# Kernel tuning notes

Measured on AMD Instinct MI355X. Metric: run time of the kernel, lower is better.

The kernel has to match this reference:

```python
import jax, jax.numpy as jnp
import numpy as np
from jax import lax

SCALES = [0.5, 0.25, 0.125, 0.0625]
D_MODEL = 256
IN_CH = 1


def setup_inputs() -> dict:
    key = jax.random.key(0)
    ks = jax.random.split(key, 16)
    x = jax.random.normal(ks[0], (2, D_MODEL, 256, 256), dtype=jnp.float32)
    m = jax.random.uniform(ks[1], (2, IN_CH, 256, 256), dtype=jnp.float32)
    s = 0.05
    Wq = jax.random.normal(ks[2], (D_MODEL, D_MODEL, 1, 1), jnp.float32) * s
    bq = jax.random.normal(ks[3], (D_MODEL,), jnp.float32) * s
    Wk = jax.random.normal(ks[4], (D_MODEL, D_MODEL, 1, 1), jnp.float32) * s
    bk = jax.random.normal(ks[5], (D_MODEL,), jnp.float32) * s
    Wv = jax.random.normal(ks[6], (D_MODEL, D_MODEL, 1, 1), jnp.float32) * s
    bv = jax.random.normal(ks[7], (D_MODEL,), jnp.float32) * s
    Wmq = jax.random.normal(ks[8], (D_MODEL, IN_CH, 1, 1), jnp.float32) * s
    bmq = jax.random.normal(ks[9], (D_MODEL,), jnp.float32) * s
    Wmk = jax.random.normal(ks[10], (D_MODEL, IN_CH, 1, 1), jnp.float32) * s
    bmk = jax.random.normal(ks[11], (D_MODEL,), jnp.float32) * s
    Wo = jax.random.normal(ks[12], (D_MODEL, D_MODEL, 3, 3), jnp.float32) * s
    bo = jax.random.normal(ks[13], (D_MODEL,), jnp.float32) * s
    return {"x": x, "m": m, "Wq": Wq, "bq": bq, "Wk": Wk, "bk": bk,
            "Wv": Wv, "bv": bv, "Wmq": Wmq, "bmq": bmq, "Wmk": Wmk, "bmk": bmk,
            "Wo": Wo, "bo": bo, "b": 1, "c": 256}


def _conv1x1(z, W, bias):
    # W: (O, I, 1, 1)
    return jnp.einsum('bihw,oi->bohw', z, W[:, :, 0, 0]) + bias[None, :, None, None]


def _forward(x, m, Wq, bq, Wk, bk, Wv, bv, Wmq, bmq, Wmk, bmk, Wo, bo, b, c):
    bt, _, h, w = x.shape  # h, w are multiples of 64 -> pad is zero
    t = bt // b
    n_scales = len(SCALES)
    d_k = c // n_scales

    q = _conv1x1(x, Wq, bq)
    k = _conv1x1(x, Wk, bk)
    v = _conv1x1(x, Wv, bv)
    mq = _conv1x1(m, Wmq, bmq)
    mk = _conv1x1(m, Wmk, bmk)

    outs = []
    for i, scale in enumerate(SCALES):
        height, width = int(h * scale), int(w * scale)
        out_h, out_w = h // height, w // width
        sl = slice(i * d_k, (i + 1) * d_k)

        def patch(z):
            # (b, t, d_k, out_h, height, out_w, width) -> (b, t*out_h*out_w, d_k*height*width)
            z = z[:, sl].reshape(b, t, d_k, out_h, height, out_w, width)
            z = z.transpose(0, 1, 3, 5, 2, 4, 6)
            return z.reshape(b, t * out_h * out_w, d_k * height * width)

        Q, K, V = patch(q), patch(k), patch(v)
        MQ, MK = patch(mq), patch(mk)
        inv_sqrt_d = 1.0 / jnp.sqrt(jnp.asarray(Q.shape[-1], jnp.float32))
        scores = jnp.einsum('bnd,bmd->bnm', Q, K) * inv_sqrt_d
        mask_scores = jnp.einsum('bnd,bmd->bnm', MQ, MK) * inv_sqrt_d
        p_attn = jax.nn.softmax(scores * mask_scores, axis=-1)
        y = jnp.einsum('bnm,bmd->bnd', p_attn, V)
        # back to (bt, d_k, h, w)
        y = y.reshape(b, t, out_h, out_w, d_k, height, width)
        y = y.transpose(0, 1, 4, 2, 5, 3, 6).reshape(bt, d_k, h, w)
        outs.append(y)

    out = jnp.concatenate(outs, axis=1)
    z = lax.conv_general_dilated(out, Wo, window_strides=(1, 1),
                                 padding=((1, 1), (1, 1)),
                                 dimension_numbers=('NCHW', 'OIHW', 'NCHW'))
    z = z + bo[None, :, None, None]
    return jnp.where(z > 0, z, 0.2 * z)  # LeakyReLU(0.2)


def reference(x, m, Wq, bq, Wk, bk, Wv, bv, Wmq, bmq, Wmk, bmk, Wo, bo, b, c):
    return _forward(x, m, Wq, bq, Wk, bk, Wv, bv, Wmq, bmq, Wmk, bmk, Wo, bo, b, c)
```

## Files before the change

kernel.cpp:

```cpp
#include <hip/hip_runtime.h>
#include <stdint.h>


typedef __attribute__((ext_vector_type(8))) short short8;
typedef __attribute__((ext_vector_type(4))) float floatx4;
typedef __attribute__((ext_vector_type(4))) unsigned int uintx4;

#define DEV static __device__ __forceinline__

DEV unsigned short f2bf(float f) {
  unsigned u = __builtin_bit_cast(unsigned, f);
  unsigned r = u + 0x7FFFu + ((u >> 16) & 1u);
  return (unsigned short)(r >> 16);
}

DEV void patch_row(int n, int sc, int lw, int& pt, int& sp0) {
  pt = n >> (2 + 2 * sc);
  int rem = n & ((4 << (2 * sc)) - 1);
  int oh = rem >> (1 + sc), ow = rem & ((2 << sc) - 1);
  sp0 = (oh << (lw + 8)) + (ow << lw);
}

__global__ void k_prep_w(const float* __restrict__ Wq, const float* __restrict__ Wk,
                         const float* __restrict__ Wv, const float* __restrict__ bq,
                         const float* __restrict__ bk, const float* __restrict__ bv,
                         const float* __restrict__ Wmq, const float* __restrict__ bmq,
                         const float* __restrict__ Wmk, const float* __restrict__ bmk,
                         unsigned short* __restrict__ wqkv, float* __restrict__ bias,
                         float* __restrict__ msc) {
  int b = blockIdx.x;
  int t = threadIdx.x;
  if (b < 768) {
    const float* src = b < 256 ? (Wq + b * 256) : (b < 512 ? (Wk + (b - 256) * 256)
                                                           : (Wv + (b - 512) * 256));
    wqkv[b * 256 + t] = f2bf(src[t]);
    if (t == 0) bias[b] = b < 256 ? bq[b] : (b < 512 ? bk[b - 256] : bv[b - 512]);
  } else {
    int sc = t >> 6, lane = t & 63;
    int ch = sc * 64 + lane;
    float a0 = Wmq[ch] * Wmk[ch];
    float a1 = Wmq[ch] * bmk[ch];
    float a2 = bmq[ch] * Wmk[ch];
    float a3 = bmq[ch] * bmk[ch];
    for (int off = 32; off; off >>= 1) {
      a0 += __shfl_xor(a0, off); a1 += __shfl_xor(a1, off);
      a2 += __shfl_xor(a2, off); a3 += __shfl_xor(a3, off);
    }
    if (lane == 0) {
      msc[sc * 4 + 0] = a0; msc[sc * 4 + 1] = a1;
      msc[sc * 4 + 2] = a2; msc[sc * 4 + 3] = a3;
    }
  }
}

__global__ void k_prep_wo(const float* __restrict__ Wo, unsigned short* __restrict__ wobf,
                          float* __restrict__ scoresG, unsigned int* __restrict__ pbuf) {
  int blk = blockIdx.x;
  if (blk < 2304) {
    int didx = blk >> 8, o = blk & 255, c = threadIdx.x;
    wobf[didx * 65536 + o * 256 + c] = f2bf(Wo[o * 2304 + c * 9 + didx]);
  } else {
    int i = (blk - 2304) * 256 + threadIdx.x;
    if (i < 559232) scoresG[i] = 0.f;
    if (i < 140032) pbuf[i] = 0u;
  }
}

__global__ __launch_bounds__(256) void k_yt(const unsigned short* __restrict__ ynat,
                                            unsigned short* __restrict__ yt) {
  __shared__ __align__(16) unsigned short tile[64][72];
  int p0 = blockIdx.x * 64, c0 = blockIdx.y * 64, t = blockIdx.z;
  int tid = threadIdx.x;
  {
    int cc = tid >> 2, pq = (tid & 3) * 16;
    const unsigned short* src = ynat + ((t * 256 + c0 + cc) * 65536 + p0 + pq);
    *(uintx4*)&tile[cc][pq] = *(const uintx4*)src;
    *(uintx4*)&tile[cc][pq + 8] = *(const uintx4*)(src + 8);
  }
  __syncthreads();
  {
    int pp = tid >> 2, cg = (tid & 3) * 16;
    __align__(16) unsigned short outv[16];
#pragma unroll
    for (int e = 0; e < 16; ++e) outv[e] = tile[cg + e][pp];
    unsigned short* dst = yt + ((t * 65536 + p0 + pp) * 256 + c0 + cg);
    *(uintx4*)dst = *(const uintx4*)&outv[0];
    *(uintx4*)(dst + 8) = *(const uintx4*)&outv[8];
  }
}

__global__ __launch_bounds__(256) void k_qkv(const float* __restrict__ x,
                                             const unsigned short* __restrict__ wqkv,
                                             const float* __restrict__ bias,
                                             unsigned short* __restrict__ qkv) {
  __shared__ __align__(16) unsigned short As[128][64];
  __shared__ __align__(16) unsigned short Bs[128][64];
  int flat = blockIdx.x + (blockIdx.y << 10);
  int lg = ((flat & 7) * 768) + (flat >> 3);
  int n_t = lg / 6, m_t = lg - n_t * 6;
  int n0 = n_t << 7, m0 = m_t << 7;
  int tid = threadIdx.x;
  int w = tid >> 6, l = tid & 63;
  int wr = w >> 1, wc = w & 1;
  int l15 = l & 15, lhi = l >> 4;
  int sr = tid >> 1, sbase = (tid & 1) * 4, r7 = sr & 7;
  const unsigned short* gA = wqkv + (m0 + sr) * 256 + sbase * 8;
  int chl = tid & 63, pseg = tid >> 6;
  int tt = n0 >> 16, pp0 = (n0 & 65535) + pseg * 32;
  const float* gB = x + ((tt * 256 + chl) * 65536 + pp0);
  floatx4 zf = {0.f, 0.f, 0.f, 0.f};
  floatx4 acc[4][4];
#pragma unroll
  for (int i = 0; i < 4; ++i)
#pragma unroll
    for (int j = 0; j < 4; ++j) acc[i][j] = zf;
  uintx4 ra[4];
  floatx4 rxb[8];
#define QLOAD(K0) { const uintx4* pa = (const uintx4*)(gA + (K0)); \
                    ra[0] = pa[0]; ra[1] = pa[1]; ra[2] = pa[2]; ra[3] = pa[3]; \
                    const float* pb = gB + (K0) * 65536; \
                    _Pragma("unroll") for (int q = 0; q < 8; ++q) \
                      rxb[q] = *(const floatx4*)(pb + q * 4); }
  QLOAD(0);
#pragma unroll
  for (int ch = 0; ch < 4; ++ch) {
    __align__(16) unsigned short tmps[32];
#pragma unroll
    for (int e = 0; e < 32; ++e) tmps[e] = f2bf(rxb[e >> 2][e & 3]);
    __syncthreads();
#pragma unroll
    for (int j = 0; j < 4; ++j)
      *(uintx4*)&As[sr][((sbase + j) ^ r7) * 8] = ra[j];
    {
      int ck = chl >> 3, cw = chl & 7;
#pragma unroll
      for (int e = 0; e < 32; ++e) {
        int p = pseg * 32 + e;
        Bs[p][((ck ^ (e & 7)) << 3) + cw] = tmps[e];
      }
    }
    __syncthreads();
    if (ch < 3) QLOAD((ch + 1) * 64);
#pragma unroll
    for (int kk = 0; kk < 2; ++kk) {
      short8 af[4], bfr[4];
#pragma unroll
      for (int f = 0; f < 4; ++f) {
        int arow = wr * 64 + f * 16 + l15;
        af[f] = *(const short8*)&As[arow][(((kk << 2) + lhi) ^ (arow & 7)) * 8];
        int brow = wc * 64 + f * 16 + l15;
        bfr[f] = *(const short8*)&Bs[brow][(((kk << 2) + lhi) ^ (brow & 7)) * 8];
      }
#pragma unroll
      for (int fm = 0; fm < 4; ++fm)
#pragma unroll
        for (int fn = 0; fn < 4; ++fn)
          acc[fm][fn] = __builtin_amdgcn_mfma_f32_16x16x32_bf16(af[fm], bfr[fn], acc[fm][fn], 0, 0, 0);
    }
  }
#undef QLOAD
#pragma unroll
  for (int fm = 0; fm < 4; ++fm) {
    int crow = m0 + wr * 64 + fm * 16 + lhi * 4;
#pragma unroll
    for (int rr = 0; rr < 4; ++rr) {
      float bv = bias[crow + rr];
#pragma unroll
      for (int fn = 0; fn < 4; ++fn) {
        int pcol = n0 + wc * 64 + fn * 16 + l15;
        int t = pcol >> 16, p = pcol & 65535;
        qkv[(t * 768 + crow + rr) * 65536 + p] = f2bf(acc[fm][fn][rr] + bv);
      }
    }
  }
}

__global__ __launch_bounds__(256) void k_gram2(const float* __restrict__ m,
                                               float* __restrict__ G) {
  __shared__ __align__(16) float Ns[32][68];
  __shared__ __align__(16) float Ms[32][68];
  int bid = blockIdx.x;
  int sc, tn, tm, z, nchunks, soff;
  if (bid < 32)      { sc = 0; tn = 0; tm = 0; z = bid;      nchunks = 8; soff = 0; }
  else if (bid < 40) { sc = 1; tn = 0; tm = 0; z = bid - 32; nchunks = 8; soff = 64; }
  else if (bid < 72) { int r = bid - 40; int tl = r >> 1; sc = 2; tn = tl >> 2; tm = tl & 3; z = r & 1; nchunks = 8; soff = 1088; }
  else               { int tl = bid - 72; sc = 3; tn = tl >> 4; tm = tl & 15; z = 0; nchunks = 4; soff = 17472; }
  int lw = 7 - sc, W = 1 << lw, N = 8 << (2 * sc);
  int kbase = z * nchunks * 64;
  int n0 = tn * 32, m0 = tm * 32;
  int tid = threadIdx.x;
  bool isA = tid < 128;
  int u = tid & 127;
  int srow = u >> 2, sslot0 = (u & 3) * 4;
  int grow = (isA ? n0 : m0) + srow;
  bool valid = grow < N;
  int pt = 0, sp0 = 0;
  if (valid) patch_row(grow, sc, lw, pt, sp0);
  int gbase = pt * 65536 + sp0;
  int trc = tid >> 4, tcc = tid & 15;
  float a00 = 0.f, a01 = 0.f, a10 = 0.f, a11 = 0.f;
  floatx4 zf = {0.f, 0.f, 0.f, 0.f};
  for (int c = 0; c < nchunks; ++c) {
    int k0 = kbase + c * 64;
    floatx4 v[4];
#pragma unroll
    for (int j = 0; j < 4; ++j) {
      v[j] = zf;
      if (valid) {
        int s = k0 + (sslot0 + j) * 4;
        int hh = s >> lw, ww = s & (W - 1);
        v[j] = *(const floatx4*)(m + gbase + (hh << 8) + ww);
      }
    }
    __syncthreads();
    float* dstrow = isA ? &Ns[srow][0] : &Ms[srow][0];
#pragma unroll
    for (int j = 0; j < 4; ++j) *(floatx4*)&dstrow[(sslot0 + j) * 4] = v[j];
    __syncthreads();
#pragma unroll 4
    for (int k = 0; k < 64; k += 4) {
      floatx4 na = *(const floatx4*)&Ns[2 * trc][k];
      floatx4 nb = *(const floatx4*)&Ns[2 * trc + 1][k];
      floatx4 ma = *(const floatx4*)&Ms[2 * tcc][k];
      floatx4 mb = *(const floatx4*)&Ms[2 * tcc + 1][k];
#pragma unroll
      for (int e = 0; e < 4; ++e) {
        a00 += na[e] * ma[e]; a01 += na[e] * mb[e];
        a10 += nb[e] * ma[e]; a11 += nb[e] * mb[e];
      }
    }
  }
  int rn = n0 + 2 * trc, rm = m0 + 2 * tcc;
  float res[2][2] = {{a00, a01}, {a10, a11}};
#pragma unroll
  for (int i = 0; i < 2; ++i)
#pragma unroll
    for (int j = 0; j < 2; ++j) {
      if (rn + i < N && rm + j < N) {
        float* dst = &G[soff + (rn + i) * N + rm + j];
        if (sc < 3) atomicAdd(dst, res[i][j]); else *dst = res[i][j];
      }
    }
}

__global__ void k_rsum(const float* __restrict__ m, float* __restrict__ rbuf) {
  int row = blockIdx.x, lane = threadIdx.x;
  int sc, n;
  if (row < 8)        { sc = 0; n = row; }
  else if (row < 40)  { sc = 1; n = row - 8; }
  else if (row < 168) { sc = 2; n = row - 40; }
  else                { sc = 3; n = row - 168; }
  int lw = 7 - sc, W = 1 << lw;
  int pt, sp0;
  patch_row(n, sc, lw, pt, sp0);
  int base = pt * 65536 + sp0;
  int S = 1 << (14 - 2 * sc);
  float acc = 0.f;
  for (int s = lane; s < S; s += 64) {
    int hh = s >> lw, ww = s & (W - 1);
    acc += m[base + (hh << 8) + ww];
  }
  for (int off = 32; off; off >>= 1) acc += __shfl_xor(acc, off);
  if (lane == 0) rbuf[row] = acc;
}

__global__ __launch_bounds__(256) void k_scores2(const unsigned short* __restrict__ qkv,
                                                 float* __restrict__ scores) {
  __shared__ __align__(16) unsigned short As[32][136];
  __shared__ __align__(16) unsigned short Bs[32][136];
  int bid = blockIdx.x;
  int sc, tn, tm, z, soff;
  if (bid < 256)      { sc = 0; tn = 0; tm = 0; z = bid;       soff = 0; }
  else                { sc = 1; tn = 0; tm = 0; z = bid - 256; soff = 64; }
  int lw = 7 - sc, W = 1 << lw, lS = 14 - 2 * sc, N = 8 << (2 * sc);
  int n0 = tn * 32, m0 = tm * 32;
  int kbase = z * 4096;
  int tid = threadIdx.x, w = tid >> 6, l = tid & 63;
  int wr = w >> 1, wc = w & 1, l15 = l & 15, lhi = l >> 4;
  floatx4 acc = {0.f, 0.f, 0.f, 0.f};
  bool isA = tid < 128;
  int u = tid & 127;
  int srow = u >> 2, sslot0 = (u & 3) * 4;
  int grow = (isA ? n0 : m0) + srow;
  int cb = (isA ? 0 : 256) + sc * 64;
  int pt = 0, sp0 = 0;
  bool valid = grow < N;
  if (valid) patch_row(grow, sc, lw, pt, sp0);
  int rowbase = (pt * 768 + cb) * 65536 + sp0;
  uintx4 zu = {0u, 0u, 0u, 0u};
  uintx4 r[4];
#define SLOAD(KS) { int kb2 = kbase + (KS) * 128; \
  _Pragma("unroll") for (int j = 0; j < 4; ++j) { \
    uintx4 v = zu; \
    if (valid) { int k = kb2 + (sslot0 + j) * 8; \
      int cl = k >> lS; int s = k & ((1 << lS) - 1); \
      int hh = s >> lw, ww = s & (W - 1); \
      v = *(const uintx4*)(qkv + rowbase + cl * 65536 + (hh << 8) + ww); } \
    r[j] = v; } }
  SLOAD(0);
  for (int ks = 0; ks < 32; ++ks) {
    __syncthreads();
    {
      unsigned short* dstrow = isA ? &As[srow][0] : &Bs[srow][0];
#pragma unroll
      for (int j = 0; j < 4; ++j) *(uintx4*)&dstrow[(sslot0 + j) * 8] = r[j];
    }
    __syncthreads();
    if (ks < 31) SLOAD(ks + 1);
#pragma unroll
    for (int kk = 0; kk < 4; ++kk) {
      short8 a = *(const short8*)&As[wr * 16 + l15][(kk * 4 + lhi) * 8];
      short8 b = *(const short8*)&Bs[wc * 16 + l15][(kk * 4 + lhi) * 8];
      acc = __builtin_amdgcn_mfma_f32_16x16x32_bf16(a, b, acc, 0, 0, 0);
    }
  }
#undef SLOAD
  int rrow = n0 + wr * 16 + lhi * 4;
  int ccol = m0 + wc * 16 + l15;
  if (ccol < N) {
#pragma unroll
    for (int rr = 0; rr < 4; ++rr)
      if (rrow + rr < N) atomicAdd(&scores[soff + (rrow + rr) * N + ccol], acc[rr]);
  }
}

__global__ __launch_bounds__(256) void k_scores_big(const unsigned short* __restrict__ qkv,
                                                    float* __restrict__ scores) {
  __shared__ __align__(16) unsigned short As[128][64];
  __shared__ __align__(16) unsigned short Bs[128][64];
  int flat = blockIdx.x;
  int lg = (flat & 7) * 20 + (flat >> 3);
  int sc, tn, tm, z, soff;
  if (lg < 32) { sc = 2; tn = 0; tm = 0; z = lg; soff = 1088; }
  else { int r = lg - 32; int tl = r >> 3; sc = 3; tn = tl >> 2; tm = tl & 3; z = r & 7; soff = 17472; }
  int N = 8 << (2 * sc);
  int lw = 7 - sc, W = 1 << lw, lS = 14 - 2 * sc;
  int n0 = tn * 128, m0 = tm * 128;
  int kbase = z * 2048;
  int tid = threadIdx.x;
  int w = tid >> 6, l = tid & 63;
  int wr = w >> 1, wc = w & 1;
  int l15 = l & 15, lhi = l >> 4;
  int sr = tid >> 1, sbase = (tid & 1) * 4, r7 = sr & 7;
  int ptA, spA, ptB, spB;
  patch_row(n0 + sr, sc, lw, ptA, spA);
  patch_row(m0 + sr, sc, lw, ptB, spB);
  int baseA = (ptA * 768 + sc * 64) * 65536 + spA;
  int baseB = (ptB * 768 + 256 + sc * 64) * 65536 + spB;
  floatx4 zf = {0.f, 0.f, 0.f, 0.f};
  floatx4 acc[4][4];
#pragma unroll
  for (int i = 0; i < 4; ++i)
#pragma unroll
    for (int j = 0; j < 4; ++j) acc[i][j] = zf;
  uintx4 ra[4], rb[4];
#define GLOAD(K0) { \
  _Pragma("unroll") for (int j = 0; j < 4; ++j) { \
    int k = kbase + (K0) + (sbase + j) * 8; \
    int cl = k >> lS; int s = k & ((1 << lS) - 1); \
    int hh = s >> lw, ww = s & (W - 1); \
    int off = cl * 65536 + (hh << 8) + ww; \
    ra[j] = *(const uintx4*)(qkv + baseA + off); \
    rb[j] = *(const uintx4*)(qkv + baseB + off); } }
  GLOAD(0);
  for (int st = 0; st < 32; ++st) {
    __syncthreads();
#pragma unroll
    for (int j = 0; j < 4; ++j) {
      *(uintx4*)&As[sr][((sbase + j) ^ r7) * 8] = ra[j];
      *(uintx4*)&Bs[sr][((sbase + j) ^ r7) * 8] = rb[j];
    }
    __syncthreads();
    if (st < 31) GLOAD((st + 1) * 64);
#pragma unroll
    for (int kk = 0; kk < 2; ++kk) {
      short8 af[4], bfr[4];
#pragma unroll
      for (int f = 0; f < 4; ++f) {
        int arow = wr * 64 + f * 16 + l15;
        af[f] = *(const short8*)&As[arow][(((kk << 2) + lhi) ^ (arow & 7)) * 8];
        int brow = wc * 64 + f * 16 + l15;
        bfr[f] = *(const short8*)&Bs[brow][(((kk << 2) + lhi) ^ (brow & 7)) * 8];
      }
#pragma unroll
      for (int fm = 0; fm < 4; ++fm)
#pragma unroll
        for (int fn = 0; fn < 4; ++fn)
          acc[fm][fn] = __builtin_amdgcn_mfma_f32_16x16x32_bf16(af[fm], bfr[fn], acc[fm][fn], 0, 0, 0);
    }
  }
#undef GLOAD
#pragma unroll
  for (int fm = 0; fm < 4; ++fm) {
    int nrow = n0 + wr * 64 + fm * 16 + lhi * 4;
#pragma unroll
    for (int rr = 0; rr < 4; ++rr) {
#pragma unroll
      for (int fn = 0; fn < 4; ++fn) {
        int mcol = m0 + wc * 64 + fn * 16 + l15;
        atomicAdd(&scores[soff + (nrow + rr) * N + mcol], acc[fm][fn][rr]);
      }
    }
  }
}

__global__ void k_softmax(const float* __restrict__ scores, const float* __restrict__ G,
                          const float* __restrict__ rbuf, const float* __restrict__ msc,
                          unsigned short* __restrict__ pbuf) {
  int row = blockIdx.x, lane = threadIdx.x;
  int sc, n, roff, soff, poff;
  if (row < 8)        { sc = 0; n = row;       roff = 0;   soff = 0;     poff = 0; }
  else if (row < 40)  { sc = 1; n = row - 8;   roff = 8;   soff = 64;    poff = 512; }
  else if (row < 168) { sc = 2; n = row - 40;  roff = 40;  soff = 1088;  poff = 1536; }
  else                { sc = 3; n = row - 168; roff = 168; soff = 17472; poff = 17920; }
  int N = 8 << (2 * sc);
  int Kpad = (sc < 2) ? 32 : N;
  float Sf = (float)(1 << (14 - 2 * sc));
  float invD = 1.0f / (float)(1 << (20 - 2 * sc));
  float alpha = msc[sc * 4 + 0], beta = msc[sc * 4 + 1];
  float gamma = msc[sc * 4 + 2], delta = msc[sc * 4 + 3];
  float rn = rbuf[roff + n];
  float vals[8];
  float mx = -1e30f;
#pragma unroll
  for (int j = 0; j < 8; ++j) {
    float v = -1e30f;
    int mcol = lane + j * 64;
    if (j * 64 < N && mcol < N) {
      float sq = scores[soff + n * N + mcol];
      float g = G[soff + n * N + mcol];
      float rm = rbuf[roff + mcol];
      v = sq * (alpha * g + beta * rn + gamma * rm + delta * Sf) * invD;
    }
    vals[j] = v;
    mx = fmaxf(mx, v);
  }
  for (int off = 32; off; off >>= 1) mx = fmaxf(mx, __shfl_xor(mx, off));
  float sum = 0.f;
#pragma unroll
  for (int j = 0; j < 8; ++j) {
    int mcol = lane + j * 64;
    float e = 0.f;
    if (j * 64 < N && mcol < N) e = __expf(vals[j] - mx);
    vals[j] = e;
    sum += e;
  }
  for (int off = 32; off; off >>= 1) sum += __shfl_xor(sum, off);
  float inv = 1.f / sum;
#pragma unroll
  for (int j = 0; j < 8; ++j) {
    int mcol = lane + j * 64;
    if (j * 64 < N && mcol < N) pbuf[poff + n * Kpad + mcol] = f2bf(vals[j] * inv);
  }
}

__global__ __launch_bounds__(256) void k_pv(const unsigned short* __restrict__ qkv,
                                            const unsigned short* __restrict__ pbuf,
                                            unsigned short* __restrict__ ynat) {
  int bid = blockIdx.x;
  int sc, bx, by;
  if (bid < 4096)      { sc = 0; bx = bid; by = 0; }
  else if (bid < 6144) { sc = 1; bx = bid - 4096; by = 0; }
  else if (bid < 8192) { int r = bid - 6144; sc = 2; bx = r >> 1; by = r & 1; }
  else                 { int r = bid - 8192; sc = 3; bx = r >> 3; by = r & 7; }
  int WR    = (sc == 0) ? 1 : (sc == 1) ? 2 : 4;
  int logWC = (sc == 0) ? 2 : (sc == 1) ? 1 : 0;
  int poff  = (sc == 0) ? 0 : (sc == 1) ? 512 : (sc == 2) ? 1536 : 17920;
  int lw = 7 - sc, W = 1 << lw;
  int lS = 14 - 2 * sc;
  int N = 8 << (2 * sc);
  int Kpad = (sc < 2) ? 32 : N;
  int WC = 1 << logWC;
  int d0 = bx * (WC * 64);
  int nb = by * (WR * 16);
  __shared__ __align__(16) unsigned short As[2][64][40];
  __shared__ __align__(16) unsigned short Bt[2][256][32];
  int tid = threadIdx.x;
  int w = tid >> 6, l = tid & 63;
  int wr = w >> logWC, wc = w & (WC - 1);
  int l15 = l & 15, lhi = l >> 4;
  floatx4 zf = {0.f, 0.f, 0.f, 0.f};
  floatx4 acc[4];
#pragma unroll
  for (int i = 0; i < 4; ++i) acc[i] = zf;
  int bmp = tid & 15;
  int dg = tid >> 4;
  bool act0 = (WC > 1) || (dg < 8);
  bool has1 = (WC == 4);
  bool doA = tid < WR * 64;
  int arow = tid >> 2, akg = (tid & 3) * 8;
  int ksteps = Kpad >> 5;
  uintx4 zu = {0u, 0u, 0u, 0u};
  int vcb = (512 + sc * 64) * 65536;
  uintx4 av = zu, lo0 = zu, hi0 = zu, lo1 = zu, hi1 = zu;
#define PLOADS(KS) { int k0 = (KS) * 32; \
    av = zu; lo0 = zu; hi0 = zu; lo1 = zu; hi1 = zu; \
    if (doA) av = *(const uintx4*)(pbuf + poff + (nb + arow) * Kpad + k0 + akg); \
    int gm0 = k0 + 2 * bmp, gm1 = gm0 + 1; \
    bool mv0 = gm0 < N, mv1 = gm1 < N; \
    int pt0 = 0, sp00 = 0, pt1 = 0, sp01 = 0; \
    if (mv0) patch_row(gm0, sc, lw, pt0, sp00); \
    if (mv1) patch_row(gm1, sc, lw, pt1, sp01); \
    { int d = d0 + dg * 8; int cl = d >> lS; int s = d & ((1 << lS) - 1); \
      int hh = s >> lw, ww = s & (W - 1); int sp = (hh << 8) + ww; \
      if (act0 && mv0) lo0 = *(const uintx4*)(qkv + pt0 * 768 * 65536 + vcb + cl * 65536 + sp00 + sp); \
      if (act0 && mv1) hi0 = *(const uintx4*)(qkv + pt1 * 768 * 65536 + vcb + cl * 65536 + sp01 + sp); } \
    if (has1) { int d = d0 + (dg + 16) * 8; int cl = d >> lS; int s = d & ((1 << lS) - 1); \
      int hh = s >> lw, ww = s & (W - 1); int sp = (hh << 8) + ww; \
      if (mv0) lo1 = *(const uintx4*)(qkv + pt0 * 768 * 65536 + vcb + cl * 65536 + sp00 + sp); \
      if (mv1) hi1 = *(const uintx4*)(qkv + pt1 * 768 * 65536 + vcb + cl * 65536 + sp01 + sp); } }
  PLOADS(0);
  for (int ks = 0; ks < ksteps; ++ks) {
    int b = ks & 1;
    if (doA) *(uintx4*)&As[b][arow][akg] = av;
    if (act0) {
      int du = dg * 8;
#pragma unroll
      for (int j = 0; j < 8; ++j) {
        int d = du + j;
        unsigned losh = (lo0[j >> 1] >> ((j & 1) * 16)) & 0xFFFFu;
        unsigned hish = (hi0[j >> 1] >> ((j & 1) * 16)) & 0xFFFFu;
        unsigned wv = losh | (hish << 16);
        int slot = (bmp >> 2) ^ ((d >> 1) & 3) ^ ((d >> 3) & 3);
        ((unsigned int*)&Bt[b][d][0])[slot * 4 + (bmp & 3)] = wv;
      }
    }
    if (has1) {
      int du = (dg + 16) * 8;
#pragma unroll
      for (int j = 0; j < 8; ++j) {
        int d = du + j;
        unsigned losh = (lo1[j >> 1] >> ((j & 1) * 16)) & 0xFFFFu;
        unsigned hish = (hi1[j >> 1] >> ((j & 1) * 16)) & 0xFFFFu;
        unsigned wv = losh | (hish << 16);
        int slot = (bmp >> 2) ^ ((d >> 1) & 3) ^ ((d >> 3) & 3);
        ((unsigned int*)&Bt[b][d][0])[slot * 4 + (bmp & 3)] = wv;
      }
    }
    __syncthreads();
    if (ks + 1 < ksteps) PLOADS(ks + 1);
    short8 a = *(const short8*)&As[b][wr * 16 + l15][lhi * 8];
#pragma unroll
    for (int fn = 0; fn < 4; ++fn) {
      int row = wc * 64 + fn * 16 + l15;
      int slot = lhi ^ ((row >> 1) & 3) ^ ((row >> 3) & 3);
      short8 bb = *(const short8*)&Bt[b][row][slot * 8];
      acc[fn] = __builtin_amdgcn_mfma_f32_16x16x32_bf16(a, bb, acc[fn], 0, 0, 0);
    }
  }
#undef PLOADS
  int nrow = nb + wr * 16 + lhi * 4;
#pragma unroll
  for (int rr = 0; rr < 4; ++rr) {
    int n = nrow + rr;
    if (n < N) {
      int pt, sp0;
      patch_row(n, sc, lw, pt, sp0);
#pragma unroll
      for (int fn = 0; fn < 4; ++fn) {
        int d = d0 + wc * 64 + fn * 16 + l15;
        int cl = d >> lS;
        int s = d & ((1 << lS) - 1);
        int hh = s >> lw, ww = s & (W - 1);
        int c = sc * 64 + cl;
        ynat[(pt * 256 + c) * 65536 + sp0 + (hh << 8) + ww] = f2bf(acc[fn][rr]);
      }
    }
  }
}

__global__ __launch_bounds__(256, 2) void k_conv(const unsigned short* __restrict__ yt,
                                                 const unsigned short* __restrict__ wo,
                                                 const float* __restrict__ bo,
                                                 float* __restrict__ out) {
  __shared__ __align__(16) unsigned short As[128][128];
  __shared__ __align__(16) unsigned short Bs[130][64];
  int flat = blockIdx.x;
  int lg = ((flat & 7) << 7) + (flat >> 3);
  int n_t = lg >> 1, m_t = lg & 1;
  int n0 = n_t << 8, m0 = m_t << 7;
  int tt = n0 >> 16, yy = (n0 >> 8) & 255;
  int tid = threadIdx.x;
  int w = tid >> 6, l = tid & 63;
  int wr = w >> 1, wc = w & 1;
  int l15 = l & 15, lhi = l >> 4;
  int a_d0 = tid >> 7, a_o0 = tid & 127;
  bool doA1 = tid < 128;
  bool doBh = tid >= 254;
  floatx4 zf = {0.f, 0.f, 0.f, 0.f};
  floatx4 acc[4][8];
#pragma unroll
  for (int i = 0; i < 4; ++i)
#pragma unroll
    for (int j = 0; j < 8; ++j) acc[i][j] = zf;
  uintx4 zu = {0u, 0u, 0u, 0u};
  uintx4 rb[4], ra0[4], ra1[4];
  const unsigned short* ybase = yt + (tt << 24);
#define CLOAD(ST) { \
    int dy = (ST) >> 3, cc = ((ST) & 7) << 5; \
    int yq = yy + dy - 1; \
    bool yv = (unsigned)yq < 256u; \
    { int xq = tid - 1; \
      if (yv && (unsigned)xq < 256u) { \
        const uintx4* p = (const uintx4*)(ybase + ((yq << 8) + xq) * 256 + cc); \
        rb[0] = p[0]; rb[1] = p[1]; rb[2] = p[2]; rb[3] = p[3]; \
      } else { rb[0] = zu; rb[1] = zu; rb[2] = zu; rb[3] = zu; } } \
    { const uintx4* p = (const uintx4*)(wo + (dy * 3 + a_d0) * 65536 + (m0 + a_o0) * 256 + cc); \
      ra0[0] = p[0]; ra0[1] = p[1]; ra0[2] = p[2]; ra0[3] = p[3]; } \
    if (doA1) { \
      const uintx4* p = (const uintx4*)(wo + (dy * 3 + 2) * 65536 + (m0 + tid) * 256 + cc); \
      ra1[0] = p[0]; ra1[1] = p[1]; ra1[2] = p[2]; ra1[3] = p[3]; \
    } else if (doBh) { \
      int xq = tid + 1; \
      if (yv && xq < 256) { \
        const uintx4* p = (const uintx4*)(ybase + ((yq << 8) + xq) * 256 + cc); \
        ra1[0] = p[0]; ra1[1] = p[1]; ra1[2] = p[2]; ra1[3] = p[3]; \
      } else { ra1[0] = zu; ra1[1] = zu; ra1[2] = zu; ra1[3] = zu; } } }
  CLOAD(0);
  for (int st = 0; st < 24; ++st) {
    __syncthreads();
    {
      int brow = tid >> 1, bhf = (tid & 1) * 4, br7 = brow & 7;
#pragma unroll
      for (int j = 0; j < 4; ++j)
        *(uintx4*)&Bs[brow][((bhf + j) ^ br7) * 8] = rb[j];
      int ao7 = a_o0 & 7;
#pragma unroll
      for (int j = 0; j < 4; ++j)
        *(uintx4*)&As[a_o0][((a_d0 * 4 + j) ^ ao7) * 8] = ra0[j];
      if (doA1) {
        int o7 = tid & 7;
#pragma unroll
        for (int j = 0; j < 4; ++j)
          *(uintx4*)&As[tid][((8 + j) ^ o7) * 8] = ra1[j];
      } else if (doBh) {
        int xh = tid + 2;
        int brow2 = xh >> 1, bhf2 = (xh & 1) * 4, br72 = brow2 & 7;
#pragma unroll
        for (int j = 0; j < 4; ++j)
          *(uintx4*)&Bs[brow2][((bhf2 + j) ^ br72) * 8] = ra1[j];
      }
    }
    __syncthreads();
    if (st < 23) CLOAD(st + 1);
#pragma unroll
    for (int dx = 0; dx < 3; ++dx) {
      short8 af[4];
#pragma unroll
      for (int f = 0; f < 4; ++f) {
        int ol = wr * 64 + f * 16 + l15;
        af[f] = *(const short8*)&As[ol][((dx * 4 + lhi) ^ (ol & 7)) * 8];
      }
#pragma unroll
      for (int fn = 0; fn < 8; ++fn) {
        int xh = wc * 128 + fn * 16 + l15 + dx;
        short8 b = *(const short8*)&Bs[xh >> 1][((((xh & 1) * 4 + lhi)) ^ ((xh >> 1) & 7)) * 8];
#pragma unroll
        for (int fm = 0; fm < 4; ++fm)
          acc[fm][fn] = __builtin_amdgcn_mfma_f32_16x16x32_bf16(af[fm], b, acc[fm][fn], 0, 0, 0);
      }
    }
  }
#undef CLOAD
#pragma unroll
  for (int fm = 0; fm < 4; ++fm) {
    int o = m0 + wr * 64 + fm * 16 + lhi * 4;
#pragma unroll
    for (int rr = 0; rr < 4; ++rr) {
      float bias = bo[o + rr];
#pragma unroll
      for (int fn = 0; fn < 8; ++fn) {
        int xcol = wc * 128 + fn * 16 + l15;
        float z = acc[fm][fn][rr] + bias;
        out[((tt * 256 + o + rr) << 16) + (yy << 8) + xcol] = z > 0.f ? z : 0.2f * z;
      }
    }
  }
}

extern "C" void kernel_launch(void* const* d_in, const int* in_sizes, int n_in,
                              void* d_out, int out_size, void* d_ws, size_t ws_size,
                              hipStream_t stream) {
  const float* x   = (const float*)d_in[0];
  const float* m   = (const float*)d_in[1];
  const float* Wq  = (const float*)d_in[2];
  const float* bq  = (const float*)d_in[3];
  const float* Wk  = (const float*)d_in[4];
  const float* bk  = (const float*)d_in[5];
  const float* Wv  = (const float*)d_in[6];
  const float* bv  = (const float*)d_in[7];
  const float* Wmq = (const float*)d_in[8];
  const float* bmq = (const float*)d_in[9];
  const float* Wmk = (const float*)d_in[10];
  const float* bmk = (const float*)d_in[11];
  const float* Wo  = (const float*)d_in[12];
  const float* bo  = (const float*)d_in[13];

  char* ws = (char*)d_ws;
  unsigned short* qkv   = (unsigned short*)(ws);
  unsigned short* ytb   = (unsigned short*)(ws + 201326592);
  unsigned short* wqkv  = (unsigned short*)(ws + 268435456);
  unsigned short* wobf  = (unsigned short*)(ws + 268828672);
  float* bias           = (float*)(ws + 270008320);
  float* msc            = (float*)(ws + 270011392);
  float* scores         = (float*)(ws + 270011456);
  float* G              = (float*)(ws + 271129920);
  float* rbuf           = (float*)(ws + 272248384);
  unsigned short* pbuf  = (unsigned short*)(ws + 272251104);
  float* out            = (float*)d_out;
  unsigned short* ynat  = (unsigned short*)d_out;

  k_prep_w<<<dim3(769), dim3(256), 0, stream>>>(Wq, Wk, Wv, bq, bk, bv, Wmq, bmq, Wmk, bmk,
                                                wqkv, bias, msc);
  k_prep_wo<<<dim3(4489), dim3(256), 0, stream>>>(Wo, wobf, scores, (unsigned int*)pbuf);
  k_qkv<<<dim3(1024, 6), dim3(256), 0, stream>>>(x, wqkv, bias, qkv);
  k_gram2<<<dim3(328), dim3(256), 0, stream>>>(m, G);
  k_rsum<<<dim3(680), dim3(64), 0, stream>>>(m, rbuf);
  k_scores2<<<dim3(320), dim3(256), 0, stream>>>(qkv, scores);
  k_scores_big<<<dim3(160), dim3(256), 0, stream>>>(qkv, scores);
  k_softmax<<<dim3(680), dim3(64), 0, stream>>>(scores, G, rbuf, msc, pbuf);
  k_pv<<<dim3(10240), dim3(256), 0, stream>>>(qkv, pbuf, ynat);
  k_yt<<<dim3(1024, 4, 2), dim3(256), 0, stream>>>(ynat, ytb);
  k_conv<<<dim3(1024), dim3(256), 0, stream>>>(ytb, wobf, bo, out);
}
```

Before: 627.2 us.

## Pre-transpose x to bf16 pixel-major and widen QKV GEMM N-tile

Adds a k_xt kernel that converts x to bf16 and transposes it to pixel-major layout, so the QKV GEMM loads contiguous 16-byte rows of B instead of doing per-element conversions and scattered scalar LDS stores. The GEMM tile grows from 128x128 to 128x256 with 4x8 accumulators per wave and launch_bounds(256,2), which increases A reuse. The trade is an extra pass over x (read fp32, write bf16) and higher register pressure. The transposed-x buffer reuses the workspace region that k_yt later overwrites.

```diff
diff --git a/kernel.cpp b/kernel.cpp
--- a/kernel.cpp
+++ b/kernel.cpp
@@ -66,6 +66,36 @@
   }
 }
 
+__global__ __launch_bounds__(256) void k_xt(const float* __restrict__ x,
+                                            unsigned short* __restrict__ xt) {
+  __shared__ __align__(16) unsigned short tile[64][72];
+  int p0 = blockIdx.x * 64, c0 = blockIdx.y * 64, t = blockIdx.z;
+  int tid = threadIdx.x;
+  {
+    int cc = tid >> 2, pq = (tid & 3) * 16;
+    const float* src = x + ((t * 256 + c0 + cc) * 65536 + p0 + pq);
+    __align__(16) unsigned short tmp[16];
+#pragma unroll
+    for (int e = 0; e < 16; e += 4) {
+      floatx4 v = *(const floatx4*)(src + e);
+      tmp[e + 0] = f2bf(v[0]); tmp[e + 1] = f2bf(v[1]);
+      tmp[e + 2] = f2bf(v[2]); tmp[e + 3] = f2bf(v[3]);
+    }
+    *(uintx4*)&tile[cc][pq] = *(const uintx4*)&tmp[0];
+    *(uintx4*)&tile[cc][pq + 8] = *(const uintx4*)&tmp[8];
+  }
+  __syncthreads();
+  {
+    int pp = tid >> 2, cg = (tid & 3) * 16;
+    __align__(16) unsigned short outv[16];
+#pragma unroll
+    for (int e = 0; e < 16; ++e) outv[e] = tile[cg + e][pp];
+    unsigned short* dst = xt + ((t * 65536 + p0 + pp) * 256 + c0 + cg);
+    *(uintx4*)dst = *(const uintx4*)&outv[0];
+    *(uintx4*)(dst + 8) = *(const uintx4*)&outv[8];
+  }
+}
+
 __global__ __launch_bounds__(256) void k_yt(const unsigned short* __restrict__ ynat,
                                             unsigned short* __restrict__ yt) {
   __shared__ __align__(16) unsigned short tile[64][72];
@@ -89,73 +119,64 @@
   }
 }
 
-__global__ __launch_bounds__(256) void k_qkv(const float* __restrict__ x,
-                                             const unsigned short* __restrict__ wqkv,
-                                             const float* __restrict__ bias,
-                                             unsigned short* __restrict__ qkv) {
+__global__ __launch_bounds__(256, 2) void k_qkv(const unsigned short* __restrict__ xt,
+                                                const unsigned short* __restrict__ wqkv,
+                                                const float* __restrict__ bias,
+                                                unsigned short* __restrict__ qkv) {
   __shared__ __align__(16) unsigned short As[128][64];
-  __shared__ __align__(16) unsigned short Bs[128][64];
-  int flat = blockIdx.x + (blockIdx.y << 10);
-  int lg = ((flat & 7) * 768) + (flat >> 3);
+  __shared__ __align__(16) unsigned short Bs[256][64];
+  int flat = blockIdx.x;
+  int lg = (flat & 7) * 384 + (flat >> 3);
   int n_t = lg / 6, m_t = lg - n_t * 6;
-  int n0 = n_t << 7, m0 = m_t << 7;
+  int n0 = n_t << 8, m0 = m_t << 7;
   int tid = threadIdx.x;
   int w = tid >> 6, l = tid & 63;
   int wr = w >> 1, wc = w & 1;
   int l15 = l & 15, lhi = l >> 4;
   int sr = tid >> 1, sbase = (tid & 1) * 4, r7 = sr & 7;
+  int b7 = tid & 7;
   const unsigned short* gA = wqkv + (m0 + sr) * 256 + sbase * 8;
-  int chl = tid & 63, pseg = tid >> 6;
-  int tt = n0 >> 16, pp0 = (n0 & 65535) + pseg * 32;
-  const float* gB = x + ((tt * 256 + chl) * 65536 + pp0);
+  const unsigned short* gB = xt + (n0 + tid) * 256;
   floatx4 zf = {0.f, 0.f, 0.f, 0.f};
-  floatx4 acc[4][4];
+  floatx4 acc[4][8];
 #pragma unroll
   for (int i = 0; i < 4; ++i)
 #pragma unroll
-    for (int j = 0; j < 4; ++j) acc[i][j] = zf;
-  uintx4 ra[4];
-  floatx4 rxb[8];
+    for (int j = 0; j < 8; ++j) acc[i][j] = zf;
+  uintx4 ra[4], rb[8];
 #define QLOAD(K0) { const uintx4* pa = (const uintx4*)(gA + (K0)); \
                     ra[0] = pa[0]; ra[1] = pa[1]; ra[2] = pa[2]; ra[3] = pa[3]; \
-                    const float* pb = gB + (K0) * 65536; \
-                    _Pragma("unroll") for (int q = 0; q < 8; ++q) \
-                      rxb[q] = *(const floatx4*)(pb + q * 4); }
+                    const uintx4* pb = (const uintx4*)(gB + (K0)); \
+                    rb[0] = pb[0]; rb[1] = pb[1]; rb[2] = pb[2]; rb[3] = pb[3]; \
+                    rb[4] = pb[4]; rb[5] = pb[5]; rb[6] = pb[6]; rb[7] = pb[7]; }
   QLOAD(0);
 #pragma unroll
   for (int ch = 0; ch < 4; ++ch) {
-    __align__(16) unsigned short tmps[32];
-#pragma unroll
-    for (int e = 0; e < 32; ++e) tmps[e] = f2bf(rxb[e >> 2][e & 3]);
     __syncthreads();
 #pragma unroll
     for (int j = 0; j < 4; ++j)
       *(uintx4*)&As[sr][((sbase + j) ^ r7) * 8] = ra[j];
-    {
-      int ck = chl >> 3, cw = chl & 7;
-#pragma unroll
-      for (int e = 0; e < 32; ++e) {
-        int p = pseg * 32 + e;
-        Bs[p][((ck ^ (e & 7)) << 3) + cw] = tmps[e];
-      }
-    }
+#pragma unroll
+    for (int j = 0; j < 8; ++j)
+      *(uintx4*)&Bs[tid][(j ^ b7) * 8] = rb[j];
     __syncthreads();
     if (ch < 3) QLOAD((ch + 1) * 64);
 #pragma unroll
     for (int kk = 0; kk < 2; ++kk) {
-      short8 af[4], bfr[4];
+      short8 af[4];
 #pragma unroll
       for (int f = 0; f < 4; ++f) {
         int arow = wr * 64 + f * 16 + l15;
         af[f] = *(const short8*)&As[arow][(((kk << 2) + lhi) ^ (arow & 7)) * 8];
-        int brow = wc * 64 + f * 16 + l15;
-        bfr[f] = *(const short8*)&Bs[brow][(((kk << 2) + lhi) ^ (brow & 7)) * 8];
-      }
-#pragma unroll
-      for (int fm = 0; fm < 4; ++fm)
-#pragma unroll
-        for (int fn = 0; fn < 4; ++fn)
-          acc[fm][fn] = __builtin_amdgcn_mfma_f32_16x16x32_bf16(af[fm], bfr[fn], acc[fm][fn], 0, 0, 0);
+      }
+#pragma unroll
+      for (int fn = 0; fn < 8; ++fn) {
+        int brow = wc * 128 + fn * 16 + l15;
+        short8 b = *(const short8*)&Bs[brow][(((kk << 2) + lhi) ^ (brow & 7)) * 8];
+#pragma unroll
+        for (int fm = 0; fm < 4; ++fm)
+          acc[fm][fn] = __builtin_amdgcn_mfma_f32_16x16x32_bf16(af[fm], b, acc[fm][fn], 0, 0, 0);
+      }
     }
   }
 #undef QLOAD
@@ -166,8 +187,8 @@
     for (int rr = 0; rr < 4; ++rr) {
       float bv = bias[crow + rr];
 #pragma unroll
-      for (int fn = 0; fn < 4; ++fn) {
-        int pcol = n0 + wc * 64 + fn * 16 + l15;
+      for (int fn = 0; fn < 8; ++fn) {
+        int pcol = n0 + wc * 128 + fn * 16 + l15;
         int t = pcol >> 16, p = pcol & 65535;
         qkv[(t * 768 + crow + rr) * 65536 + p] = f2bf(acc[fm][fn][rr] + bv);
       }
@@ -698,7 +719,7 @@
 
   char* ws = (char*)d_ws;
   unsigned short* qkv   = (unsigned short*)(ws);
-  unsigned short* ytb   = (unsigned short*)(ws + 201326592);
+  unsigned short* xtb   = (unsigned short*)(ws + 201326592);
   unsigned short* wqkv  = (unsigned short*)(ws + 268435456);
   unsigned short* wobf  = (unsigned short*)(ws + 268828672);
   float* bias           = (float*)(ws + 270008320);
@@ -713,13 +734,14 @@
   k_prep_w<<<dim3(769), dim3(256), 0, stream>>>(Wq, Wk, Wv, bq, bk, bv, Wmq, bmq, Wmk, bmk,
                                                 wqkv, bias, msc);
   k_prep_wo<<<dim3(4489), dim3(256), 0, stream>>>(Wo, wobf, scores, (unsigned int*)pbuf);
-  k_qkv<<<dim3(1024, 6), dim3(256), 0, stream>>>(x, wqkv, bias, qkv);
+  k_xt<<<dim3(1024, 4, 2), dim3(256), 0, stream>>>(x, xtb);
+  k_qkv<<<dim3(3072), dim3(256), 0, stream>>>(xtb, wqkv, bias, qkv);
   k_gram2<<<dim3(328), dim3(256), 0, stream>>>(m, G);
   k_rsum<<<dim3(680), dim3(64), 0, stream>>>(m, rbuf);
   k_scores2<<<dim3(320), dim3(256), 0, stream>>>(qkv, scores);
   k_scores_big<<<dim3(160), dim3(256), 0, stream>>>(qkv, scores);
   k_softmax<<<dim3(680), dim3(64), 0, stream>>>(scores, G, rbuf, msc, pbuf);
   k_pv<<<dim3(10240), dim3(256), 0, stream>>>(qkv, pbuf, ynat);
-  k_yt<<<dim3(1024, 4, 2), dim3(256), 0, stream>>>(ynat, ytb);
-  k_conv<<<dim3(1024), dim3(256), 0, stream>>>(ytb, wobf, bo, out);
-}
+  k_yt<<<dim3(1024, 4, 2), dim3(256), 0, stream>>>(ynat, xtb);
+  k_conv<<<dim3(1024), dim3(256), 0, stream>>>(xtb, wobf, bo, out);
+}
```

Measured after the change: 577.3 us. 1.09x faster.
